# Performance work log

Measured on AMD Instinct MI355X. Metric: run time of the kernel, lower is better.

The kernel has to match this reference:

```python
import jax, jax.numpy as jnp
import numpy as np

N = 100000   # nodes
E = 1600000  # edges per meta-path graph
D_IN = 256
H = 4        # num_heads
F = 32       # out_feats per head
D_HID = H * F  # 128
D_SEM = 128  # semantic attention hidden dim
C = 8        # output classes
NEG_SLOPE = 0.2


def setup_inputs() -> dict:
    key = jax.random.key(0)
    ks = jax.random.split(key, 24)
    inp = {
        "x": jax.random.normal(ks[0], (N, D_IN), dtype=jnp.float32),
        "src0": jax.random.randint(ks[1], (E,), 0, N),
        "dst0": jax.random.randint(ks[2], (E,), 0, N),
        "ew0": jax.random.uniform(ks[3], (E,), dtype=jnp.float32),
        "src1": jax.random.randint(ks[4], (E,), 0, N),
        "dst1": jax.random.randint(ks[5], (E,), 0, N),
        "ew1": jax.random.uniform(ks[6], (E,), dtype=jnp.float32),
    }
    s_in = 1.0 / np.sqrt(D_IN)
    s_f = 1.0 / np.sqrt(F)
    s_h = 1.0 / np.sqrt(D_HID)
    s_s = 1.0 / np.sqrt(D_SEM)
    # GAT params for meta-path 0 and 1 (tuple feat -> separate fc_src/fc_dst)
    inp["Wsrc0"] = jax.random.normal(ks[7], (D_IN, D_HID), dtype=jnp.float32) * s_in
    inp["Wdst0"] = jax.random.normal(ks[8], (D_IN, D_HID), dtype=jnp.float32) * s_in
    inp["al0"] = jax.random.normal(ks[9], (H, F), dtype=jnp.float32) * s_f
    inp["ar0"] = jax.random.normal(ks[10], (H, F), dtype=jnp.float32) * s_f
    inp["b0"] = jnp.zeros((D_HID,), dtype=jnp.float32)
    inp["Wsrc1"] = jax.random.normal(ks[11], (D_IN, D_HID), dtype=jnp.float32) * s_in
    inp["Wdst1"] = jax.random.normal(ks[12], (D_IN, D_HID), dtype=jnp.float32) * s_in
    inp["al1"] = jax.random.normal(ks[13], (H, F), dtype=jnp.float32) * s_f
    inp["ar1"] = jax.random.normal(ks[14], (H, F), dtype=jnp.float32) * s_f
    inp["b1"] = jnp.zeros((D_HID,), dtype=jnp.float32)
    # Semantic attention: Linear(D_HID->128) -> tanh -> Linear(128->1, no bias)
    inp["Wp1"] = jax.random.normal(ks[15], (D_HID, D_SEM), dtype=jnp.float32) * s_h
    inp["bp1"] = jnp.zeros((D_SEM,), dtype=jnp.float32)
    inp["Wp2"] = jax.random.normal(ks[16], (D_SEM, 1), dtype=jnp.float32) * s_s
    # Prediction head
    inp["Wo"] = jax.random.normal(ks[17], (D_HID, C), dtype=jnp.float32) * s_h
    inp["bo"] = jnp.zeros((C,), dtype=jnp.float32)
    return inp


def gat_conv(x, Wsrc, Wdst, al, ar, b, src, dst, ew):
    # feat_src/feat_dst: [N, H, F]
    fs = (x @ Wsrc).reshape(N, H, F)
    fd = (x @ Wdst).reshape(N, H, F)
    el = jnp.einsum('nhf,hf->nh', fs, al)  # [N, H]
    er = jnp.einsum('nhf,hf->nh', fd, ar)  # [N, H]
    e = jax.nn.leaky_relu(el[src] + er[dst], negative_slope=NEG_SLOPE)  # [E, H]
    a = jax.nn.sigmoid(e) * ew[:, None]  # [E, H]  (sigmoid attention * edge_weight)
    m = fs[src] * a[:, :, None]  # [E, H, F]
    out = jax.ops.segment_sum(m, dst, num_segments=N)  # [N, H, F]
    out = out + b.reshape(1, H, F)
    return jax.nn.elu(out).reshape(N, H * F)


def semantic_attention(z, Wp1, bp1, Wp2):
    # z: [N, P, D_HID]
    w = jnp.tanh(z @ Wp1 + bp1) @ Wp2  # [N, P, 1]
    w = w.mean(axis=0)                  # [P, 1]
    beta = jax.nn.softmax(w, axis=0)    # softmax over meta-paths
    return (beta[None] * z).sum(axis=1)  # [N, D_HID]


def reference(x, src0, dst0, ew0, src1, dst1, ew1,
              Wsrc0, Wdst0, al0, ar0, b0,
              Wsrc1, Wdst1, al1, ar1, b1,
              Wp1, bp1, Wp2, Wo, bo):
    z0 = gat_conv(x, Wsrc0, Wdst0, al0, ar0, b0, src0, dst0, ew0)
    z1 = gat_conv(x, Wsrc1, Wdst1, al1, ar1, b1, src1, dst1, ew1)
    z = jnp.stack([z0, z1], axis=1)  # [N, 2, H*F]
    h = semantic_attention(z, Wp1, bp1, Wp2)  # [N, H*F]
    return h @ Wo + bo  # [N, C]
```

## Files before the change

kernel.cpp:

```cpp
#include <hip/hip_runtime.h>
#include <hip/hip_fp16.h>
#include <math.h>

#define N_NODES 100000
#define N_EDGES 1600000
#define D_IN    256
#define D_HID   128
#define NH      4
#define NF      32
#define D_SEM   128
#define NC      8
#define NEG_SLOPE 0.2f
#define BUCKET  64
#define BIN_SHIFT 9
#define BINS    196
#define BIN_CAP 9216
#define CHUNK   8192

typedef _Float16 half8 __attribute__((ext_vector_type(8)));
typedef float    floatx4 __attribute__((ext_vector_type(4)));

struct BinArgs {
    const int*   src[2];
    const int*   dst[2];
    const float* ew[2];
    int*         gcur[2];
    uint2*       binned[2];
};
struct BucketArgs {
    const int*   gcur[2];
    const uint2* binned[2];
    int*         cnt[2];
    unsigned*    edg[2];
};

__global__ void prep_fold(const float* __restrict__ Ws0, const float* __restrict__ al0,
                          const float* __restrict__ Wd0, const float* __restrict__ ar0,
                          const float* __restrict__ Ws1, const float* __restrict__ al1,
                          const float* __restrict__ Wd1, const float* __restrict__ ar1,
                          float* __restrict__ WF) {
    int d = threadIdx.x;
    for (int p = 0; p < 2; ++p) {
        const float* Ws = p ? Ws1 : Ws0;
        const float* al = p ? al1 : al0;
        const float* Wd = p ? Wd1 : Wd0;
        const float* ar = p ? ar1 : ar0;
        for (int h = 0; h < NH; ++h) {
            float se = 0.f, sr = 0.f;
            for (int f = 0; f < NF; ++f) {
                se = fmaf(Ws[d*D_HID + h*NF + f], al[h*NF + f], se);
                sr = fmaf(Wd[d*D_HID + h*NF + f], ar[h*NF + f], sr);
            }
            WF[d*16 + p*8 + h]     = se;
            WF[d*16 + p*8 + 4 + h] = sr;
        }
    }
}

__global__ __launch_bounds__(256) void prep_tr(const float* __restrict__ Ws0,
                                               const float* __restrict__ Ws1,
                                               const float* __restrict__ Wp1,
                                               __half* __restrict__ WT0,
                                               __half* __restrict__ WT1,
                                               __half* __restrict__ WP1T) {
    int g = blockIdx.x * 256 + threadIdx.x;
    if (g < 32768) {
        int c = g >> 8, k = g & 255;
        WT0[g] = __float2half_rn(Ws0[k*D_HID + c]);
    } else if (g < 65536) {
        int g2 = g - 32768;
        int c = g2 >> 8, k = g2 & 255;
        WT1[g2] = __float2half_rn(Ws1[k*D_HID + c]);
    } else {
        int g2 = g - 65536;
        int c = g2 >> 7, k = g2 & 127;
        WP1T[g2] = __float2half_rn(Wp1[k*D_SEM + c]);
    }
}

__global__ __launch_bounds__(256) void er_el_kernel(const float* __restrict__ x,
                                                    const float* __restrict__ WF,
                                                    float* __restrict__ eler,
                                                    __half* __restrict__ XH) {
    __shared__ float xs[16][260];
    __shared__ float wfs[4096];
    int tid = threadIdx.x;
    #pragma unroll
    for (int i = 0; i < 16; ++i) wfs[tid + i*256] = WF[tid + i*256];
    int n0 = blockIdx.x * 16;
    #pragma unroll
    for (int i = 0; i < 4; ++i) {
        int id = tid + i*256;
        int r = id >> 6, c = (id & 63) << 2;
        *(float4*)&xs[r][c] = *(const float4*)&x[(size_t)(n0 + r)*D_IN + c];
    }
    __syncthreads();
    int node = tid >> 4, c = tid & 15;
    float s = 0.f;
    #pragma unroll 8
    for (int k = 0; k < 256; ++k) s = fmaf(xs[node][k], wfs[k*16 + c], s);
    int p = c >> 3, e = (c >> 2) & 1, h = c & 3;
    eler[(p*2 + e)*400000 + (n0 + node)*4 + h] = s;

    #pragma unroll
    for (int i = 0; i < 4; ++i) {
        int id = tid + i*256;
        int r = id >> 6, c4 = (id & 63) << 2;
        float4 v = *(const float4*)&xs[r][c4];
        __half2 h0 = __floats2half2_rn(v.x, v.y);
        __half2 h1 = __floats2half2_rn(v.z, v.w);
        uint2 pk; pk.x = *(unsigned*)&h0; pk.y = *(unsigned*)&h1;
        *(uint2*)&XH[(size_t)(n0 + r)*D_IN + c4] = pk;
    }
}

__global__ __launch_bounds__(256) void gemm_fs_mfma(const __half* __restrict__ XH,
                                                    const __half* __restrict__ WT,
                                                    __half* __restrict__ FS) {
    __shared__ unsigned short xs[64][64];
    __shared__ unsigned short ws[128][64];
    int tid = threadIdx.x;
    int row0 = blockIdx.x * 64;
    int wid = tid >> 6, lane = tid & 63;
    int wm = wid >> 1, wn = wid & 1;
    int lr = lane & 15, lk = lane >> 4;

    floatx4 acc[2][4];
    #pragma unroll
    for (int m = 0; m < 2; ++m)
        #pragma unroll
        for (int n = 0; n < 4; ++n) acc[m][n] = (floatx4){0.f, 0.f, 0.f, 0.f};

    for (int k0 = 0; k0 < D_IN; k0 += 64) {
        #pragma unroll
        for (int i = 0; i < 2; ++i) {
            int id = tid + i*256;
            int r = id >> 3, c8 = (id & 7) << 3;
            int grow = row0 + r;
            uint4 pk = make_uint4(0u, 0u, 0u, 0u);
            if (grow < N_NODES) pk = *(const uint4*)&XH[(size_t)grow*D_IN + k0 + c8];
            int cc = (((c8 >> 3) ^ (r & 7)) << 3);
            *(uint4*)&xs[r][cc] = pk;
        }
        #pragma unroll
        for (int i = 0; i < 8; ++i) {
            int id = tid + i*256;
            int col = id >> 4, c4 = (id & 15) << 2;
            uint2 pk = *(const uint2*)&WT[col*256 + k0 + c4];
            int cc = (((c4 >> 3) ^ (col & 7)) << 3) + (c4 & 7);
            *(uint2*)&ws[col][cc] = pk;
        }
        __syncthreads();
        #pragma unroll
        for (int kk = 0; kk < 2; ++kk) {
            int ksub = kk*4 + lk;
            half8 a[2], b[4];
            #pragma unroll
            for (int m = 0; m < 2; ++m) {
                int r = wm*32 + m*16 + lr;
                a[m] = *(half8*)&xs[r][((ksub ^ (r & 7)) << 3)];
            }
            #pragma unroll
            for (int n = 0; n < 4; ++n) {
                int c = wn*64 + n*16 + lr;
                b[n] = *(half8*)&ws[c][((ksub ^ (c & 7)) << 3)];
            }
            #pragma unroll
            for (int m = 0; m < 2; ++m)
                #pragma unroll
                for (int n = 0; n < 4; ++n)
                    acc[m][n] = __builtin_amdgcn_mfma_f32_16x16x32_f16(a[m], b[n], acc[m][n], 0, 0, 0);
        }
        __syncthreads();
    }

    unsigned short* outs = &ws[0][0];
    #pragma unroll
    for (int m = 0; m < 2; ++m)
        #pragma unroll
        for (int n = 0; n < 4; ++n) {
            int col = wn*64 + n*16 + lr;
            #pragma unroll
            for (int r4 = 0; r4 < 4; ++r4) {
                int rr = wm*32 + m*16 + lk*4 + r4;
                __half hv = __float2half_rn(acc[m][n][r4]);
                outs[rr*128 + col] = *(unsigned short*)&hv;
            }
        }
    __syncthreads();
    #pragma unroll
    for (int i = 0; i < 8; ++i) {
        int id = tid + i*256;
        int r = id >> 5, c4 = (id & 31) << 2;
        int grow = row0 + r;
        if (grow < N_NODES)
            *(uint2*)&FS[(size_t)grow*D_HID + c4] = *(uint2*)&outs[r*128 + c4];
    }
}

__global__ __launch_bounds__(1024) void bin_kernel(BinArgs A) {
    __shared__ uint2 stage[CHUNK];
    __shared__ unsigned char binof[CHUNK];
    __shared__ int bcnt[256], boff[256], gbase[256], brun[256];
    int P = blockIdx.y;
    const int*   src = A.src[P];
    const int*   dst = A.dst[P];
    const float* ew  = A.ew[P];
    int*         gcur = A.gcur[P];
    uint2*       binned = A.binned[P];

    int tid = threadIdx.x;
    int c0 = blockIdx.x * CHUNK;
    int C = N_EDGES - c0; if (C > CHUNK) C = CHUNK;
    if (C <= 0) return;

    if (tid < 256) bcnt[tid] = 0;
    __syncthreads();
    for (int j = tid; j < C; j += 1024)
        atomicAdd(&bcnt[dst[c0 + j] >> BIN_SHIFT], 1);
    __syncthreads();

    int v = (tid < 256) ? bcnt[tid] : 0;
    if (tid < 256) boff[tid] = v;
    __syncthreads();
    for (int o = 1; o < 256; o <<= 1) {
        int u = (tid < 256 && tid >= o) ? boff[tid - o] : 0;
        __syncthreads();
        if (tid < 256) boff[tid] += u;
        __syncthreads();
    }
    if (tid < 256) {
        boff[tid] -= v;
        brun[tid] = 0;
        if (tid < BINS) gbase[tid] = v ? atomicAdd(&gcur[tid], v) : 0;
    }
    __syncthreads();

    for (int j = tid; j < C; j += 1024) {
        int e = c0 + j;
        int d = dst[e];
        int b = d >> BIN_SHIFT;
        unsigned q = (unsigned)(ew[e] * 32767.f + 0.5f);
        int p = atomicAdd(&brun[b], 1);
        int sl = boff[b] + p;
        stage[sl] = make_uint2(((unsigned)src[e] << 15) | q, (unsigned)d);
        binof[sl] = (unsigned char)b;
    }
    __syncthreads();

    for (int j = tid; j < C; j += 1024) {
        int b = binof[j];
        int off = gbase[b] + (j - boff[b]);
        if (off < BIN_CAP) binned[b * BIN_CAP + off] = stage[j];
    }
}

__global__ __launch_bounds__(1024) void bucket_kernel(BucketArgs A) {
    __shared__ unsigned buck[256 * BUCKET];
    __shared__ int lcnt[256];
    int P = blockIdx.y;
    const int*   gcur   = A.gcur[P];
    const uint2* binned = A.binned[P];
    int*         cnt    = A.cnt[P];
    unsigned*    edg    = A.edg[P];

    int tid = threadIdx.x;
    int nb = blockIdx.x;
    int b  = nb >> 1;
    int n0 = nb << 8;
    int lo = (nb & 1) << 8;
    if (tid < 256) lcnt[tid] = 0;
    __syncthreads();

    int cE = gcur[b]; if (cE > BIN_CAP) cE = BIN_CAP;
    int bn0 = b << BIN_SHIFT;
    for (int j = tid; j < cE; j += 1024) {
        uint2 r = binned[b * BIN_CAP + j];
        int w = ((int)r.y - bn0) - lo;
        if ((unsigned)w < 256u) {
            int p = atomicAdd(&lcnt[w], 1);
            if (p < BUCKET) buck[(w << 6) + p] = r.x;
        }
    }
    __syncthreads();

    const uint4* b4 = (const uint4*)buck;
    uint4* e4 = (uint4*)edg;
    for (int i = tid; i < 256 * BUCKET / 4; i += 1024) {
        int node = n0 + (i >> 4);
        int used = lcnt[i >> 4];
        if (node < N_NODES && ((i & 15) << 2) < used)
            e4[((size_t)node << 4) + (i & 15)] = b4[i];
    }
    if (tid < 256) {
        int node = n0 + tid;
        if (node < N_NODES) cnt[node] = lcnt[tid] < BUCKET ? lcnt[tid] : BUCKET;
    }
}

__global__ __launch_bounds__(256) void agg_kernel(const __half* __restrict__ FS,
                                                  const float* __restrict__ el,
                                                  const float* __restrict__ er,
                                                  const int* __restrict__ cnt,
                                                  const unsigned* __restrict__ edg,
                                                  const float* __restrict__ bias,
                                                  __half* __restrict__ zh) {
    int wv = (blockIdx.x * 256 + threadIdx.x) >> 6;
    int lane = threadIdx.x & 63;
    if (wv >= N_NODES) return;
    int q  = lane >> 4;
    int ql = lane & 15;
    int hh = lane & 3;
    float erh = er[wv*4 + hh];
    int cn = cnt[wv];
    if (cn > BUCKET) cn = BUCKET;
    int beg = wv << 6;
    const __half* fsq = FS + (ql << 3);

    float4 a0 = make_float4(0.f,0.f,0.f,0.f);
    float4 a1 = make_float4(0.f,0.f,0.f,0.f);

    int nIt = (cn + 15) >> 4;
    for (int it = 0; it < nIt; ++it) {
        int jb = it << 4;
        int sl = jb + (lane >> 2);
        int slc = sl < cn ? sl : cn - 1;
        unsigned w = edg[beg + slc];
        int s = (int)(w >> 15);
        float a = (float)(w & 32767u) * (1.f / 32767.f);
        float v = el[s*4 + hh] + erh;
        v = v > 0.f ? v : NEG_SLOPE * v;
        a = a * __builtin_amdgcn_rcpf(1.f + __expf(-v));
        a = sl < cn ? a : 0.f;
        #pragma unroll
        for (int u = 0; u < 4; ++u) {
            int e = (u << 2) + q;
            int su = jb + e;
            int ssrc = __shfl(s, e << 2);
            uint4 raw = make_uint4(0u, 0u, 0u, 0u);
            if (su < cn) raw = *(const uint4*)&fsq[(size_t)ssrc * D_HID];
            float av = __shfl(a, (e << 2) | (ql >> 2));
            float2 f0 = __half22float2(*(__half2*)&raw.x);
            float2 f1 = __half22float2(*(__half2*)&raw.y);
            float2 f2 = __half22float2(*(__half2*)&raw.z);
            float2 f3 = __half22float2(*(__half2*)&raw.w);
            a0.x = fmaf(f0.x, av, a0.x); a0.y = fmaf(f0.y, av, a0.y);
            a0.z = fmaf(f1.x, av, a0.z); a0.w = fmaf(f1.y, av, a0.w);
            a1.x = fmaf(f2.x, av, a1.x); a1.y = fmaf(f2.y, av, a1.y);
            a1.z = fmaf(f3.x, av, a1.z); a1.w = fmaf(f3.y, av, a1.w);
        }
    }

    #pragma unroll
    for (int o = 16; o < 64; o <<= 1) {
        a0.x += __shfl_xor(a0.x, o); a0.y += __shfl_xor(a0.y, o);
        a0.z += __shfl_xor(a0.z, o); a0.w += __shfl_xor(a0.w, o);
        a1.x += __shfl_xor(a1.x, o); a1.y += __shfl_xor(a1.y, o);
        a1.z += __shfl_xor(a1.z, o); a1.w += __shfl_xor(a1.w, o);
    }

    if (q < 2) {
        int c = (ql << 3) + (q << 2);
        float4 r = q ? a1 : a0;
        float4 bv = *(const float4*)&bias[c];
        r.x += bv.x; r.y += bv.y; r.z += bv.z; r.w += bv.w;
        r.x = r.x > 0.f ? r.x : expm1f(r.x);
        r.y = r.y > 0.f ? r.y : expm1f(r.y);
        r.z = r.z > 0.f ? r.z : expm1f(r.z);
        r.w = r.w > 0.f ? r.w : expm1f(r.w);
        __half2 h0 = __floats2half2_rn(r.x, r.y);
        __half2 h1 = __floats2half2_rn(r.z, r.w);
        uint2 pk; pk.x = *(unsigned*)&h0; pk.y = *(unsigned*)&h1;
        *(uint2*)&zh[(size_t)wv*D_HID + c] = pk;
    }
}

__global__ __launch_bounds__(256) void sem_mfma(const __half* __restrict__ zh0,
                                                const __half* __restrict__ zh1,
                                                const __half* __restrict__ WP1T,
                                                const float* __restrict__ bp1,
                                                const float* __restrict__ Wp2,
                                                float* __restrict__ wsum) {
    __shared__ unsigned short zs[64][128];
    __shared__ unsigned short ps[128][128];
    __shared__ float red[4];
    const __half* z = blockIdx.y ? zh1 : zh0;
    int tid = threadIdx.x;
    int row0 = blockIdx.x * 64;
    int wid = tid >> 6, lane = tid & 63;
    int wm = wid >> 1, wn = wid & 1;
    int lr = lane & 15, lk = lane >> 4;

    #pragma unroll
    for (int i = 0; i < 4; ++i) {
        int id = tid + i*256;
        int r = id >> 4, ch = id & 15;
        int grow = row0 + r;
        uint4 pk = make_uint4(0u, 0u, 0u, 0u);
        if (grow < N_NODES) pk = *(const uint4*)&z[(size_t)grow*D_HID + (ch << 3)];
        *(uint4*)&zs[r][((ch ^ (r & 7)) << 3)] = pk;
    }
    #pragma unroll
    for (int i = 0; i < 16; ++i) {
        int id = tid + i*256;
        int c = id >> 5, k4 = (id & 31) << 2;
        uint2 pk = *(const uint2*)&WP1T[c*128 + k4];
        int cc = (((k4 >> 3) ^ (c & 7)) << 3) + (k4 & 7);
        *(uint2*)&ps[c][cc] = pk;
    }
    __syncthreads();

    floatx4 acc[2][4];
    #pragma unroll
    for (int m = 0; m < 2; ++m)
        #pragma unroll
        for (int n = 0; n < 4; ++n) acc[m][n] = (floatx4){0.f, 0.f, 0.f, 0.f};

    #pragma unroll
    for (int kk = 0; kk < 4; ++kk) {
        int ksub = kk*4 + lk;
        half8 a[2], b[4];
        #pragma unroll
        for (int m = 0; m < 2; ++m) {
            int r = wm*32 + m*16 + lr;
            a[m] = *(half8*)&zs[r][((ksub ^ (r & 7)) << 3)];
        }
        #pragma unroll
        for (int n = 0; n < 4; ++n) {
            int c = wn*64 + n*16 + lr;
            b[n] = *(half8*)&ps[c][((ksub ^ (c & 7)) << 3)];
        }
        #pragma unroll
        for (int m = 0; m < 2; ++m)
            #pragma unroll
            for (int n = 0; n < 4; ++n)
                acc[m][n] = __builtin_amdgcn_mfma_f32_16x16x32_f16(a[m], b[n], acc[m][n], 0, 0, 0);
    }

    float s = 0.f;
    #pragma unroll
    for (int m = 0; m < 2; ++m)
        #pragma unroll
        for (int n = 0; n < 4; ++n) {
            int col = wn*64 + n*16 + lr;
            float bp = bp1[col];
            float w2 = Wp2[col];
            #pragma unroll
            for (int r4 = 0; r4 < 4; ++r4) {
                int grow = row0 + wm*32 + m*16 + lk*4 + r4;
                if (grow < N_NODES) {
                    float v = acc[m][n][r4] + bp;
                    float t = 1.f - 2.f / (__expf(2.f*v) + 1.f);
                    s = fmaf(t, w2, s);
                }
            }
        }
    #pragma unroll
    for (int o = 1; o < 64; o <<= 1) s += __shfl_xor(s, o);
    if (lane == 0) red[wid] = s;
    __syncthreads();
    if (tid == 0) atomicAdd(&wsum[blockIdx.y], red[0] + red[1] + red[2] + red[3]);
}

__global__ __launch_bounds__(256) void final_kernel(const __half* __restrict__ zh0,
                                                    const __half* __restrict__ zh1,
                                                    const float* __restrict__ Wo,
                                                    const float* __restrict__ bo,
                                                    const float* __restrict__ wsum,
                                                    float* __restrict__ out) {
    __shared__ float z0s[32][132];
    __shared__ float z1s[32][132];
    __shared__ float wos[128*8];
    __shared__ float bos[8];
    int tid = threadIdx.x;
    int n0 = blockIdx.x * 32;
    #pragma unroll
    for (int i = 0; i < 4; ++i) wos[tid + i*256] = Wo[tid + i*256];
    if (tid < 8) bos[tid] = bo[tid];
    #pragma unroll
    for (int i = 0; i < 2; ++i) {
        int id = tid + i*256;
        int r = id >> 4, c8 = (id & 15) << 3;
        uint4 p0 = *(const uint4*)&zh0[(size_t)(n0 + r)*D_HID + c8];
        uint4 p1 = *(const uint4*)&zh1[(size_t)(n0 + r)*D_HID + c8];
        float2 q0 = __half22float2(*(__half2*)&p0.x);
        float2 q1 = __half22float2(*(__half2*)&p0.y);
        float2 q2 = __half22float2(*(__half2*)&p0.z);
        float2 q3 = __half22float2(*(__half2*)&p0.w);
        *(float4*)&z0s[r][c8]     = make_float4(q0.x, q0.y, q1.x, q1.y);
        *(float4*)&z0s[r][c8 + 4] = make_float4(q2.x, q2.y, q3.x, q3.y);
        q0 = __half22float2(*(__half2*)&p1.x);
        q1 = __half22float2(*(__half2*)&p1.y);
        q2 = __half22float2(*(__half2*)&p1.z);
        q3 = __half22float2(*(__half2*)&p1.w);
        *(float4*)&z1s[r][c8]     = make_float4(q0.x, q0.y, q1.x, q1.y);
        *(float4*)&z1s[r][c8 + 4] = make_float4(q2.x, q2.y, q3.x, q3.y);
    }
    __syncthreads();

    float w0 = wsum[0] * (1.f / N_NODES), w1 = wsum[1] * (1.f / N_NODES);
    float m = fmaxf(w0, w1);
    float e0 = __expf(w0 - m), e1 = __expf(w1 - m);
    float b0 = e0 / (e0 + e1), b1 = 1.f - b0;

    int node = tid >> 3, c = tid & 7;
    float s = bos[c];
    #pragma unroll 8
    for (int k = 0; k < 128; ++k) {
        float hk = b0 * z0s[node][k] + b1 * z1s[node][k];
        s = fmaf(hk, wos[k*8 + c], s);
    }
    out[(n0 + node)*NC + c] = s;
}

extern "C" void kernel_launch(void* const* d_in, const int* in_sizes, int n_in,
                              void* d_out, int out_size, void* d_ws, size_t ws_size,
                              hipStream_t stream) {
    const float* x     = (const float*)d_in[0];
    const int*   src0  = (const int*)  d_in[1];
    const int*   dst0  = (const int*)  d_in[2];
    const float* ew0   = (const float*)d_in[3];
    const int*   src1  = (const int*)  d_in[4];
    const int*   dst1  = (const int*)  d_in[5];
    const float* ew1   = (const float*)d_in[6];
    const float* Wsrc0 = (const float*)d_in[7];
    const float* Wdst0 = (const float*)d_in[8];
    const float* al0   = (const float*)d_in[9];
    const float* ar0   = (const float*)d_in[10];
    const float* b0    = (const float*)d_in[11];
    const float* Wsrc1 = (const float*)d_in[12];
    const float* Wdst1 = (const float*)d_in[13];
    const float* al1   = (const float*)d_in[14];
    const float* ar1   = (const float*)d_in[15];
    const float* b1    = (const float*)d_in[16];
    const float* Wp1   = (const float*)d_in[17];
    const float* bp1   = (const float*)d_in[18];
    const float* Wp2   = (const float*)d_in[19];
    const float* Wo    = (const float*)d_in[20];
    const float* bo    = (const float*)d_in[21];
    float* out = (float*)d_out;

    float*    ws     = (float*)d_ws;
    __half*   FS     = (__half*)ws;
    __half*   ZH0    = (__half*)(ws + 6400000);
    __half*   ZH1    = (__half*)(ws + 12800000);
    __half*   XH     = (__half*)(ws + 19200000);
    float*    ELER   = ws + 32000000;
    float*    WF     = ELER + 1600000;
    float*    WSUM   = WF + 4096;
    __half*   WT0    = (__half*)(WSUM + 8);
    __half*   WT1    = (__half*)((float*)WT0 + 16384);
    __half*   WP1T   = (__half*)((float*)WT1 + 16384);
    int*      CNT0   = (int*)((float*)WP1T + 8192);
    int*      CNT1   = CNT0  + 100000;
    int*      GCUR0  = CNT1  + 100000;
    int*      GCUR1  = GCUR0 + 256;
    unsigned* EDG0   = (unsigned*)(GCUR1 + 256);
    uint2*    BINNED0= (uint2*)(EDG0 + 6400000);
    float*    endser = (float*)BINNED0 + 2*(size_t)BINS*BIN_CAP;
    unsigned* EDG1   = (unsigned*)endser;
    uint2*    BINNED1= (uint2*)(EDG1 + 6400000);
    size_t fused_bytes = (size_t)((float*)BINNED1 + 2*(size_t)BINS*BIN_CAP - ws) * 4;
    bool fused = ws_size >= fused_bytes;
    if (!fused) { EDG1 = EDG0; BINNED1 = BINNED0; }

    hipMemsetAsync(GCUR0, 0, sizeof(int)*512, stream);
    hipMemsetAsync(WSUM, 0, sizeof(float)*4, stream);

    prep_fold<<<1, 256, 0, stream>>>(Wsrc0, al0, Wdst0, ar0, Wsrc1, al1, Wdst1, ar1, WF);
    prep_tr<<<320, 256, 0, stream>>>(Wsrc0, Wsrc1, Wp1, WT0, WT1, WP1T);
    er_el_kernel<<<N_NODES/16, 256, 0, stream>>>(x, WF, ELER, XH);

    int nchunks = (N_EDGES + CHUNK - 1) / CHUNK;
    if (fused) {
        BinArgs ba = {{src0, src1}, {dst0, dst1}, {ew0, ew1},
                      {GCUR0, GCUR1}, {BINNED0, BINNED1}};
        bin_kernel<<<dim3(nchunks, 2), 1024, 0, stream>>>(ba);
        BucketArgs ka = {{GCUR0, GCUR1}, {BINNED0, BINNED1},
                         {CNT0, CNT1}, {EDG0, EDG1}};
        bucket_kernel<<<dim3(2*BINS, 2), 1024, 0, stream>>>(ka);
        gemm_fs_mfma<<<(N_NODES + 63)/64, 256, 0, stream>>>(XH, WT0, FS);
        agg_kernel<<<(N_NODES*64)/256, 256, 0, stream>>>(FS, ELER, ELER + 400000, CNT0, EDG0, b0, ZH0);
        gemm_fs_mfma<<<(N_NODES + 63)/64, 256, 0, stream>>>(XH, WT1, FS);
        agg_kernel<<<(N_NODES*64)/256, 256, 0, stream>>>(FS, ELER + 800000, ELER + 1200000, CNT1, EDG1, b1, ZH1);
    } else {
        BinArgs ba0 = {{src0, src0}, {dst0, dst0}, {ew0, ew0},
                       {GCUR0, GCUR0}, {BINNED0, BINNED0}};
        BucketArgs ka0 = {{GCUR0, GCUR0}, {BINNED0, BINNED0},
                          {CNT0, CNT0}, {EDG0, EDG0}};
        bin_kernel<<<dim3(nchunks, 1), 1024, 0, stream>>>(ba0);
        bucket_kernel<<<dim3(2*BINS, 1), 1024, 0, stream>>>(ka0);
        gemm_fs_mfma<<<(N_NODES + 63)/64, 256, 0, stream>>>(XH, WT0, FS);
        agg_kernel<<<(N_NODES*64)/256, 256, 0, stream>>>(FS, ELER, ELER + 400000, CNT0, EDG0, b0, ZH0);
        BinArgs ba1 = {{src1, src1}, {dst1, dst1}, {ew1, ew1},
                       {GCUR1, GCUR1}, {BINNED0, BINNED0}};
        BucketArgs ka1 = {{GCUR1, GCUR1}, {BINNED0, BINNED0},
                          {CNT1, CNT1}, {EDG0, EDG0}};
        bin_kernel<<<dim3(nchunks, 1), 1024, 0, stream>>>(ba1);
        bucket_kernel<<<dim3(2*BINS, 1), 1024, 0, stream>>>(ka1);
        gemm_fs_mfma<<<(N_NODES + 63)/64, 256, 0, stream>>>(XH, WT1, FS);
        agg_kernel<<<(N_NODES*64)/256, 256, 0, stream>>>(FS, ELER + 800000, ELER + 1200000, CNT1, EDG0, b1, ZH1);
    }

    dim3 semgrid((N_NODES + 63)/64, 2);
    sem_mfma<<<semgrid, 256, 0, stream>>>(ZH0, ZH1, WP1T, bp1, Wp2, WSUM);
    final_kernel<<<N_NODES/32, 256, 0, stream>>>(ZH0, ZH1, Wo, bo, WSUM, out);
}
```

Before: 580.1 us.

## Fuse fp16 conversion, both source GEMMs and attention logits into one MFMA kernel

Replaces the separate er/el kernel, the fp16 copy of x and the two per-metapath source GEMMs with one kernel. It converts x to fp16 in shared memory, multiplies it against a concatenated weight matrix holding both Wsrc matrices plus folded Wdst·ar columns, and writes FS0 and FS1. The el logits come from a shuffle reduction of the fp32 accumulators with al, and the er logits come from an extra MFMA column block. This removes the XH round trip, one read of x, two extra launches and a second FS pass. In exchange it uses a much larger shared-memory footprint (about 67 KB), which can lower occupancy, and er is now computed from fp16 inputs.

New measurement: 549.8 us. 1.05x faster.

```diff
diff --git a/kernel.cpp b/kernel.cpp
--- a/kernel.cpp
+++ b/kernel.cpp
@@ -34,167 +34,189 @@
     unsigned*    edg[2];
 };
 
-__global__ void prep_fold(const float* __restrict__ Ws0, const float* __restrict__ al0,
-                          const float* __restrict__ Wd0, const float* __restrict__ ar0,
-                          const float* __restrict__ Ws1, const float* __restrict__ al1,
-                          const float* __restrict__ Wd1, const float* __restrict__ ar1,
-                          float* __restrict__ WF) {
-    int d = threadIdx.x;
-    for (int p = 0; p < 2; ++p) {
-        const float* Ws = p ? Ws1 : Ws0;
-        const float* al = p ? al1 : al0;
-        const float* Wd = p ? Wd1 : Wd0;
-        const float* ar = p ? ar1 : ar0;
-        for (int h = 0; h < NH; ++h) {
-            float se = 0.f, sr = 0.f;
-            for (int f = 0; f < NF; ++f) {
-                se = fmaf(Ws[d*D_HID + h*NF + f], al[h*NF + f], se);
-                sr = fmaf(Wd[d*D_HID + h*NF + f], ar[h*NF + f], sr);
-            }
-            WF[d*16 + p*8 + h]     = se;
-            WF[d*16 + p*8 + 4 + h] = sr;
-        }
-    }
-}
-
-__global__ __launch_bounds__(256) void prep_tr(const float* __restrict__ Ws0,
-                                               const float* __restrict__ Ws1,
-                                               const float* __restrict__ Wp1,
-                                               __half* __restrict__ WT0,
-                                               __half* __restrict__ WT1,
-                                               __half* __restrict__ WP1T) {
+__global__ __launch_bounds__(256) void prep(const float* __restrict__ Ws0,
+                                            const float* __restrict__ Ws1,
+                                            const float* __restrict__ Wd0,
+                                            const float* __restrict__ ar0,
+                                            const float* __restrict__ Wd1,
+                                            const float* __restrict__ ar1,
+                                            const float* __restrict__ Wp1,
+                                            __half* __restrict__ WTA,
+                                            __half* __restrict__ WP1T) {
     int g = blockIdx.x * 256 + threadIdx.x;
     if (g < 32768) {
-        int c = g >> 8, k = g & 255;
-        WT0[g] = __float2half_rn(Ws0[k*D_HID + c]);
+        int col = g >> 8, k = g & 255;
+        WTA[(size_t)col*256 + k] = __float2half_rn(Ws0[k*D_HID + col]);
     } else if (g < 65536) {
         int g2 = g - 32768;
-        int c = g2 >> 8, k = g2 & 255;
-        WT1[g2] = __float2half_rn(Ws1[k*D_HID + c]);
-    } else {
+        int col = g2 >> 8, k = g2 & 255;
+        WTA[(size_t)(128 + col)*256 + k] = __float2half_rn(Ws1[k*D_HID + col]);
+    } else if (g < 69632) {
         int g2 = g - 65536;
+        int j = g2 >> 8, k = g2 & 255;
+        float s = 0.f;
+        if (j < 8) {
+            int p = j >> 2, h = j & 3;
+            const float* Wd = p ? Wd1 : Wd0;
+            const float* ar = p ? ar1 : ar0;
+            for (int f = 0; f < NF; ++f)
+                s = fmaf(Wd[k*D_HID + h*NF + f], ar[h*NF + f], s);
+        }
+        WTA[(size_t)(256 + j)*256 + k] = __float2half_rn(s);
+    } else if (g < 86016) {
+        int g2 = g - 69632;
         int c = g2 >> 7, k = g2 & 127;
         WP1T[g2] = __float2half_rn(Wp1[k*D_SEM + c]);
     }
 }
 
-__global__ __launch_bounds__(256) void er_el_kernel(const float* __restrict__ x,
-                                                    const float* __restrict__ WF,
-                                                    float* __restrict__ eler,
-                                                    __half* __restrict__ XH) {
-    __shared__ float xs[16][260];
-    __shared__ float wfs[4096];
-    int tid = threadIdx.x;
-    #pragma unroll
-    for (int i = 0; i < 16; ++i) wfs[tid + i*256] = WF[tid + i*256];
-    int n0 = blockIdx.x * 16;
-    #pragma unroll
-    for (int i = 0; i < 4; ++i) {
-        int id = tid + i*256;
-        int r = id >> 6, c = (id & 63) << 2;
-        *(float4*)&xs[r][c] = *(const float4*)&x[(size_t)(n0 + r)*D_IN + c];
-    }
-    __syncthreads();
-    int node = tid >> 4, c = tid & 15;
-    float s = 0.f;
-    #pragma unroll 8
-    for (int k = 0; k < 256; ++k) s = fmaf(xs[node][k], wfs[k*16 + c], s);
-    int p = c >> 3, e = (c >> 2) & 1, h = c & 3;
-    eler[(p*2 + e)*400000 + (n0 + node)*4 + h] = s;
-
-    #pragma unroll
-    for (int i = 0; i < 4; ++i) {
-        int id = tid + i*256;
-        int r = id >> 6, c4 = (id & 63) << 2;
-        float4 v = *(const float4*)&xs[r][c4];
-        __half2 h0 = __floats2half2_rn(v.x, v.y);
-        __half2 h1 = __floats2half2_rn(v.z, v.w);
-        uint2 pk; pk.x = *(unsigned*)&h0; pk.y = *(unsigned*)&h1;
-        *(uint2*)&XH[(size_t)(n0 + r)*D_IN + c4] = pk;
-    }
-}
-
-__global__ __launch_bounds__(256) void gemm_fs_mfma(const __half* __restrict__ XH,
-                                                    const __half* __restrict__ WT,
-                                                    __half* __restrict__ FS) {
-    __shared__ unsigned short xs[64][64];
-    __shared__ unsigned short ws[128][64];
+__global__ __launch_bounds__(256) void fs_all(const float* __restrict__ x,
+                                              const __half* __restrict__ WTA,
+                                              const float* __restrict__ al0,
+                                              const float* __restrict__ al1,
+                                              __half* __restrict__ FS0,
+                                              __half* __restrict__ FS1,
+                                              float* __restrict__ eler) {
+    __shared__ unsigned short xs[64][256];
+    __shared__ unsigned short wsB[272][64];
     int tid = threadIdx.x;
     int row0 = blockIdx.x * 64;
     int wid = tid >> 6, lane = tid & 63;
-    int wm = wid >> 1, wn = wid & 1;
     int lr = lane & 15, lk = lane >> 4;
 
-    floatx4 acc[2][4];
-    #pragma unroll
-    for (int m = 0; m < 2; ++m)
+    #pragma unroll
+    for (int i = 0; i < 8; ++i) {
+        int id = tid + i*256;
+        int r = id >> 5, c8 = (id & 31) << 3;
+        int grow = row0 + r;
+        float4 v0 = make_float4(0.f,0.f,0.f,0.f), v1 = v0;
+        if (grow < N_NODES) {
+            v0 = *(const float4*)&x[(size_t)grow*D_IN + c8];
+            v1 = *(const float4*)&x[(size_t)grow*D_IN + c8 + 4];
+        }
+        __half2 h0 = __floats2half2_rn(v0.x, v0.y);
+        __half2 h1 = __floats2half2_rn(v0.z, v0.w);
+        __half2 h2 = __floats2half2_rn(v1.x, v1.y);
+        __half2 h3 = __floats2half2_rn(v1.z, v1.w);
+        uint4 pk;
+        pk.x = *(unsigned*)&h0; pk.y = *(unsigned*)&h1;
+        pk.z = *(unsigned*)&h2; pk.w = *(unsigned*)&h3;
+        int ch = c8 >> 3;
+        *(uint4*)&xs[r][((ch ^ (r & 7)) << 3)] = pk;
+    }
+
+    floatx4 acc[4][4];
+    floatx4 acc4[4];
+    #pragma unroll
+    for (int m = 0; m < 4; ++m) {
+        acc4[m] = (floatx4){0.f, 0.f, 0.f, 0.f};
         #pragma unroll
         for (int n = 0; n < 4; ++n) acc[m][n] = (floatx4){0.f, 0.f, 0.f, 0.f};
-
-    for (int k0 = 0; k0 < D_IN; k0 += 64) {
-        #pragma unroll
-        for (int i = 0; i < 2; ++i) {
-            int id = tid + i*256;
-            int r = id >> 3, c8 = (id & 7) << 3;
-            int grow = row0 + r;
-            uint4 pk = make_uint4(0u, 0u, 0u, 0u);
-            if (grow < N_NODES) pk = *(const uint4*)&XH[(size_t)grow*D_IN + k0 + c8];
-            int cc = (((c8 >> 3) ^ (r & 7)) << 3);
-            *(uint4*)&xs[r][cc] = pk;
-        }
-        #pragma unroll
-        for (int i = 0; i < 8; ++i) {
+    }
+
+    for (int kc = 0; kc < 4; ++kc) {
+        #pragma unroll
+        for (int i = 0; i < 17; ++i) {
             int id = tid + i*256;
             int col = id >> 4, c4 = (id & 15) << 2;
-            uint2 pk = *(const uint2*)&WT[col*256 + k0 + c4];
+            uint2 pk = *(const uint2*)&WTA[(size_t)col*256 + kc*64 + c4];
             int cc = (((c4 >> 3) ^ (col & 7)) << 3) + (c4 & 7);
-            *(uint2*)&ws[col][cc] = pk;
+            *(uint2*)&wsB[col][cc] = pk;
         }
         __syncthreads();
         #pragma unroll
         for (int kk = 0; kk < 2; ++kk) {
-            int ksub = kk*4 + lk;
-            half8 a[2], b[4];
-            #pragma unroll
-            for (int m = 0; m < 2; ++m) {
-                int r = wm*32 + m*16 + lr;
-                a[m] = *(half8*)&xs[r][((ksub ^ (r & 7)) << 3)];
+            int kl = kk*4 + lk;
+            int kg = kc*8 + kl;
+            half8 a[4], b[5];
+            #pragma unroll
+            for (int m = 0; m < 4; ++m) {
+                int r = m*16 + lr;
+                a[m] = *(half8*)&xs[r][((kg ^ (r & 7)) << 3)];
             }
             #pragma unroll
             for (int n = 0; n < 4; ++n) {
-                int c = wn*64 + n*16 + lr;
-                b[n] = *(half8*)&ws[c][((ksub ^ (c & 7)) << 3)];
-            }
-            #pragma unroll
-            for (int m = 0; m < 2; ++m)
+                int c = wid*64 + n*16 + lr;
+                b[n] = *(half8*)&wsB[c][((kl ^ (c & 7)) << 3)];
+            }
+            if (wid == 0) {
+                int c = 256 + lr;
+                b[4] = *(half8*)&wsB[c][((kl ^ (c & 7)) << 3)];
+            }
+            #pragma unroll
+            for (int m = 0; m < 4; ++m)
                 #pragma unroll
                 for (int n = 0; n < 4; ++n)
                     acc[m][n] = __builtin_amdgcn_mfma_f32_16x16x32_f16(a[m], b[n], acc[m][n], 0, 0, 0);
+            if (wid == 0) {
+                #pragma unroll
+                for (int m = 0; m < 4; ++m)
+                    acc4[m] = __builtin_amdgcn_mfma_f32_16x16x32_f16(a[m], b[4], acc4[m], 0, 0, 0);
+            }
         }
         __syncthreads();
     }
 
-    unsigned short* outs = &ws[0][0];
-    #pragma unroll
-    for (int m = 0; m < 2; ++m)
-        #pragma unroll
-        for (int n = 0; n < 4; ++n) {
-            int col = wn*64 + n*16 + lr;
+    {
+        int p = wid >> 1;
+        const float* al = p ? al1 : al0;
+        int h0 = (wid & 1) * 2;
+        float av00 = al[h0*NF + lr],     av01 = al[h0*NF + 16 + lr];
+        float av10 = al[(h0+1)*NF + lr], av11 = al[(h0+1)*NF + 16 + lr];
+        #pragma unroll
+        for (int m = 0; m < 4; ++m)
             #pragma unroll
             for (int r4 = 0; r4 < 4; ++r4) {
-                int rr = wm*32 + m*16 + lk*4 + r4;
+                float s0 = acc[m][0][r4]*av00 + acc[m][1][r4]*av01;
+                float s1 = acc[m][2][r4]*av10 + acc[m][3][r4]*av11;
+                #pragma unroll
+                for (int o = 1; o < 16; o <<= 1) {
+                    s0 += __shfl_xor(s0, o);
+                    s1 += __shfl_xor(s1, o);
+                }
+                int row = row0 + m*16 + lk*4 + r4;
+                if (lr == 0 && row < N_NODES) {
+                    eler[(p*2)*400000 + row*4 + h0]     = s0;
+                    eler[(p*2)*400000 + row*4 + h0 + 1] = s1;
+                }
+            }
+    }
+    if (wid == 0 && lr < 8) {
+        int p = lr >> 2, h = lr & 3;
+        #pragma unroll
+        for (int m = 0; m < 4; ++m)
+            #pragma unroll
+            for (int r4 = 0; r4 < 4; ++r4) {
+                int row = row0 + m*16 + lk*4 + r4;
+                if (row < N_NODES)
+                    eler[(p*2+1)*400000 + row*4 + h] = acc4[m][r4];
+            }
+    }
+
+    __syncthreads();
+    #pragma unroll
+    for (int n = 0; n < 4; ++n) {
+        int col = wid*64 + n*16 + lr;
+        #pragma unroll
+        for (int m = 0; m < 4; ++m)
+            #pragma unroll
+            for (int r4 = 0; r4 < 4; ++r4) {
+                int rr = m*16 + lk*4 + r4;
                 __half hv = __float2half_rn(acc[m][n][r4]);
-                outs[rr*128 + col] = *(unsigned short*)&hv;
-            }
-        }
+                xs[rr][col] = *(unsigned short*)&hv;
+            }
+    }
     __syncthreads();
     #pragma unroll
     for (int i = 0; i < 8; ++i) {
         int id = tid + i*256;
-        int r = id >> 5, c4 = (id & 31) << 2;
+        int r = id >> 5, c8 = (id & 31) << 3;
         int grow = row0 + r;
-        if (grow < N_NODES)
-            *(uint2*)&FS[(size_t)grow*D_HID + c4] = *(uint2*)&outs[r*128 + c4];
+        if (grow < N_NODES) {
+            uint4 pk = *(uint4*)&xs[r][c8];
+            if (c8 < 128) *(uint4*)&FS0[(size_t)grow*D_HID + c8]       = pk;
+            else          *(uint4*)&FS1[(size_t)grow*D_HID + c8 - 128] = pk;
+        }
     }
 }
 
@@ -541,16 +563,14 @@
     float* out = (float*)d_out;
 
     float*    ws     = (float*)d_ws;
-    __half*   FS     = (__half*)ws;
-    __half*   ZH0    = (__half*)(ws + 6400000);
-    __half*   ZH1    = (__half*)(ws + 12800000);
-    __half*   XH     = (__half*)(ws + 19200000);
-    float*    ELER   = ws + 32000000;
-    float*    WF     = ELER + 1600000;
-    float*    WSUM   = WF + 4096;
-    __half*   WT0    = (__half*)(WSUM + 8);
-    __half*   WT1    = (__half*)((float*)WT0 + 16384);
-    __half*   WP1T   = (__half*)((float*)WT1 + 16384);
+    __half*   FS0    = (__half*)ws;
+    __half*   FS1    = (__half*)(ws + 6400000);
+    __half*   ZH0    = (__half*)(ws + 12800000);
+    __half*   ZH1    = (__half*)(ws + 19200000);
+    float*    ELER   = ws + 25600000;
+    float*    WSUM   = ELER + 1600000;
+    __half*   WTA    = (__half*)(WSUM + 8);
+    __half*   WP1T   = (__half*)((float*)WTA + 34816);
     int*      CNT0   = (int*)((float*)WP1T + 8192);
     int*      CNT1   = CNT0  + 100000;
     int*      GCUR0  = CNT1  + 100000;
@@ -567,9 +587,8 @@
     hipMemsetAsync(GCUR0, 0, sizeof(int)*512, stream);
     hipMemsetAsync(WSUM, 0, sizeof(float)*4, stream);
 
-    prep_fold<<<1, 256, 0, stream>>>(Wsrc0, al0, Wdst0, ar0, Wsrc1, al1, Wdst1, ar1, WF);
-    prep_tr<<<320, 256, 0, stream>>>(Wsrc0, Wsrc1, Wp1, WT0, WT1, WP1T);
-    er_el_kernel<<<N_NODES/16, 256, 0, stream>>>(x, WF, ELER, XH);
+    prep<<<336, 256, 0, stream>>>(Wsrc0, Wsrc1, Wdst0, ar0, Wdst1, ar1, Wp1, WTA, WP1T);
+    fs_all<<<(N_NODES + 63)/64, 256, 0, stream>>>(x, WTA, al0, al1, FS0, FS1, ELER);
 
     int nchunks = (N_EDGES + CHUNK - 1) / CHUNK;
     if (fused) {
@@ -579,10 +598,8 @@
         BucketArgs ka = {{GCUR0, GCUR1}, {BINNED0, BINNED1},
                          {CNT0, CNT1}, {EDG0, EDG1}};
         bucket_kernel<<<dim3(2*BINS, 2), 1024, 0, stream>>>(ka);
-        gemm_fs_mfma<<<(N_NODES + 63)/64, 256, 0, stream>>>(XH, WT0, FS);
-        agg_kernel<<<(N_NODES*64)/256, 256, 0, stream>>>(FS, ELER, ELER + 400000, CNT0, EDG0, b0, ZH0);
-        gemm_fs_mfma<<<(N_NODES + 63)/64, 256, 0, stream>>>(XH, WT1, FS);
-        agg_kernel<<<(N_NODES*64)/256, 256, 0, stream>>>(FS, ELER + 800000, ELER + 1200000, CNT1, EDG1, b1, ZH1);
+        agg_kernel<<<(N_NODES*64)/256, 256, 0, stream>>>(FS0, ELER, ELER + 400000, CNT0, EDG0, b0, ZH0);
+        agg_kernel<<<(N_NODES*64)/256, 256, 0, stream>>>(FS1, ELER + 800000, ELER + 1200000, CNT1, EDG1, b1, ZH1);
     } else {
         BinArgs ba0 = {{src0, src0}, {dst0, dst0}, {ew0, ew0},
                        {GCUR0, GCUR0}, {BINNED0, BINNED0}};
@@ -590,16 +607,14 @@
                           {CNT0, CNT0}, {EDG0, EDG0}};
         bin_kernel<<<dim3(nchunks, 1), 1024, 0, stream>>>(ba0);
         bucket_kernel<<<dim3(2*BINS, 1), 1024, 0, stream>>>(ka0);
-        gemm_fs_mfma<<<(N_NODES + 63)/64, 256, 0, stream>>>(XH, WT0, FS);
-        agg_kernel<<<(N_NODES*64)/256, 256, 0, stream>>>(FS, ELER, ELER + 400000, CNT0, EDG0, b0, ZH0);
+        agg_kernel<<<(N_NODES*64)/256, 256, 0, stream>>>(FS0, ELER, ELER + 400000, CNT0, EDG0, b0, ZH0);
         BinArgs ba1 = {{src1, src1}, {dst1, dst1}, {ew1, ew1},
                        {GCUR1, GCUR1}, {BINNED0, BINNED0}};
         BucketArgs ka1 = {{GCUR1, GCUR1}, {BINNED0, BINNED0},
                           {CNT1, CNT1}, {EDG0, EDG0}};
         bin_kernel<<<dim3(nchunks, 1), 1024, 0, stream>>>(ba1);
         bucket_kernel<<<dim3(2*BINS, 1), 1024, 0, stream>>>(ka1);
-        gemm_fs_mfma<<<(N_NODES + 63)/64, 256, 0, stream>>>(XH, WT1, FS);
-        agg_kernel<<<(N_NODES*64)/256, 256, 0, stream>>>(FS, ELER + 800000, ELER + 1200000, CNT1, EDG0, b1, ZH1);
+        agg_kernel<<<(N_NODES*64)/256, 256, 0, stream>>>(FS1, ELER + 800000, ELER + 1200000, CNT1, EDG0, b1, ZH1);
     }
 
     dim3 semgrid((N_NODES + 63)/64, 2);
```
